# Optimization experiments

Measured on AMD Instinct MI355X. Metric: run time of the kernel, lower is better.

Reference implementation:

```python
import jax, jax.numpy as jnp
import numpy as np

N = 50000
E = 800000
EPS = 1e-5


def graph_conv(x, src, dst, ew, W_rel, b_rel, W_root):
    # PyG GraphConv (aggr='add'): lin_rel(sum_j e_ij * x_j) + lin_root(x_i)
    msg = x[src] * ew[:, None]                      # [E, F_in]
    agg = jax.ops.segment_sum(msg, dst, num_segments=N)  # [N, F_in]
    return agg @ W_rel.T + b_rel + x @ W_root.T


def batchnorm_relu(h, gamma, beta):
    mu = jnp.mean(h, axis=0)
    var = jnp.mean(jnp.square(h - mu), axis=0)
    hn = (h - mu) * jax.lax.rsqrt(var + EPS)
    return jax.nn.relu(hn * gamma + beta)


def setup_inputs() -> dict:
    key = jax.random.key(0)
    ks = jax.random.split(key, 16)
    d_in, h, d_out = 128, 256, 64

    def lin(k, fo, fi):
        return jax.random.normal(k, (fo, fi), jnp.float32) * (1.0 / np.sqrt(fi))

    return {
        "x": jax.random.normal(ks[0], (N, d_in), jnp.float32),
        "edge_index": jax.random.randint(ks[1], (2, E), 0, N, jnp.int32),
        "edge_weight": jax.random.uniform(ks[2], (E,), jnp.float32),
        "Wr0": lin(ks[3], h, d_in), "br0": jnp.zeros((h,), jnp.float32), "Wt0": lin(ks[4], h, d_in),
        "g0": jnp.ones((h,), jnp.float32), "be0": jnp.zeros((h,), jnp.float32),
        "Wr1": lin(ks[5], h, h), "br1": jnp.zeros((h,), jnp.float32), "Wt1": lin(ks[6], h, h),
        "g1": jnp.ones((h,), jnp.float32), "be1": jnp.zeros((h,), jnp.float32),
        "Wr2": lin(ks[7], d_out, h), "br2": jnp.zeros((d_out,), jnp.float32), "Wt2": lin(ks[8], d_out, h),
    }


def reference(x, edge_index, edge_weight, Wr0, br0, Wt0, g0, be0,
              Wr1, br1, Wt1, g1, be1, Wr2, br2, Wt2):
    src, dst = edge_index[0], edge_index[1]
    h = graph_conv(x, src, dst, edge_weight, Wr0, br0, Wt0)
    h = batchnorm_relu(h, g0, be0)
    h = graph_conv(h, src, dst, edge_weight, Wr1, br1, Wt1)
    h = batchnorm_relu(h, g1, be1)
    return graph_conv(h, src, dst, edge_weight, Wr2, br2, Wt2)
```

## Files before the change

### kernel.cpp

```cpp
#include <hip/hip_runtime.h>
#include <cstddef>
#include <cstdint>

#define SCAN_B 512

using bf16x8 = __attribute__((ext_vector_type(8))) short;
using f32x4  = __attribute__((ext_vector_type(4))) float;

__device__ __forceinline__ unsigned short f2bf(float f) {
    unsigned int u = __builtin_bit_cast(unsigned int, f);
    return (unsigned short)((u + 0x7FFFu + ((u >> 16) & 1u)) >> 16);
}
__device__ __forceinline__ float bf2f(unsigned short b) {
    unsigned int u = ((unsigned int)b) << 16;
    return __builtin_bit_cast(float, u);
}
__device__ __forceinline__ float i2f(int i) { return __builtin_bit_cast(float, i); }
__device__ __forceinline__ float u2f(unsigned int u) { return __builtin_bit_cast(float, u); }
__device__ __forceinline__ void gload_lds16(const void* g, void* l) {
    __builtin_amdgcn_global_load_lds((const __attribute__((address_space(1))) void*)g,
                                     (__attribute__((address_space(3))) void*)l, 16, 0, 0);
}

__global__ void hist_conv_k(const int* __restrict__ dst, int* __restrict__ counts,
                            int* __restrict__ rank, int E, int histBlocks,
                            const float* __restrict__ x, const float* __restrict__ Wr0,
                            const float* __restrict__ Wt0, const float* __restrict__ Wr1,
                            const float* __restrict__ Wt1, const float* __restrict__ Wr2,
                            const float* __restrict__ Wt2, unsigned short* __restrict__ x_bf,
                            unsigned short* __restrict__ Wr0b, unsigned short* __restrict__ Wt0b,
                            unsigned short* __restrict__ Wr1b, unsigned short* __restrict__ Wt1b,
                            unsigned short* __restrict__ Wr2b, unsigned short* __restrict__ Wt2b,
                            int n4x) {
    if ((int)blockIdx.x < histBlocks) {
        int e = blockIdx.x * 256 + threadIdx.x;
        if (e < E) rank[e] = atomicAdd(&counts[dst[e]], 1);
        return;
    }
    int j = (blockIdx.x - histBlocks) * 256 + threadIdx.x;
    const float* s;
    unsigned short* d;
    if (j < n4x) { s = x; d = x_bf; }
    else {
        j -= n4x;
        if (j < 8192) { s = Wr0; d = Wr0b; }
        else { j -= 8192;
        if (j < 8192) { s = Wt0; d = Wt0b; }
        else { j -= 8192;
        if (j < 16384) { s = Wr1; d = Wr1b; }
        else { j -= 16384;
        if (j < 16384) { s = Wt1; d = Wt1b; }
        else { j -= 16384;
        if (j < 4096) { s = Wr2; d = Wr2b; }
        else { j -= 4096;
        if (j >= 4096) return;
        s = Wt2; d = Wt2b; } } } } }
    }
    float4 v = reinterpret_cast<const float4*>(s)[j];
    ushort4 o;
    o.x = f2bf(v.x); o.y = f2bf(v.y); o.z = f2bf(v.z); o.w = f2bf(v.w);
    reinterpret_cast<ushort4*>(d)[j] = o;
}

__global__ void scan1_k(const int* __restrict__ counts, int* __restrict__ partial,
                        int* __restrict__ blocksum, int Nn) {
    __shared__ int sh[SCAN_B];
    int i = blockIdx.x * SCAN_B + threadIdx.x;
    int v = (i < Nn) ? counts[i] : 0;
    sh[threadIdx.x] = v;
    __syncthreads();
    for (int off = 1; off < SCAN_B; off <<= 1) {
        int t = (threadIdx.x >= (unsigned)off) ? sh[threadIdx.x - off] : 0;
        __syncthreads();
        sh[threadIdx.x] += t;
        __syncthreads();
    }
    if (i < Nn) partial[i] = sh[threadIdx.x];
    if (threadIdx.x == SCAN_B - 1) blocksum[blockIdx.x] = sh[threadIdx.x];
}

__global__ void scan2_k(int* __restrict__ blocksum, int nb) {
    __shared__ int sh[256];
    int v = (threadIdx.x < (unsigned)nb) ? blocksum[threadIdx.x] : 0;
    sh[threadIdx.x] = v;
    __syncthreads();
    for (int off = 1; off < 256; off <<= 1) {
        int t = (threadIdx.x >= (unsigned)off) ? sh[threadIdx.x - off] : 0;
        __syncthreads();
        sh[threadIdx.x] += t;
        __syncthreads();
    }
    if (threadIdx.x < (unsigned)nb) blocksum[threadIdx.x] = sh[threadIdx.x];
}

__global__ void scan3_k(const int* __restrict__ partial, const int* __restrict__ blocksum,
                        int* __restrict__ offsets, int Nn) {
    int i = blockIdx.x * SCAN_B + threadIdx.x;
    if (i >= Nn) return;
    int add = (blockIdx.x > 0) ? blocksum[blockIdx.x - 1] : 0;
    offsets[i + 1] = partial[i] + add;
    if (i == 0) offsets[0] = 0;
}

__global__ void fill2_k(const int* __restrict__ src, const int* __restrict__ dst,
                        const float* __restrict__ ew, const int* __restrict__ offsets,
                        const int* __restrict__ rank, int2* __restrict__ e_sw, int E) {
    int e = blockIdx.x * blockDim.x + threadIdx.x;
    if (e >= E) return;
    int d = dst[e];
    int pos = offsets[d] + rank[e];
    e_sw[pos] = make_int2(src[e], __builtin_bit_cast(int, ew[e]));
}

template<int F>
__global__ void gather_bf_k(const unsigned short* __restrict__ x, const int* __restrict__ offsets,
                            const int2* __restrict__ e_sw, unsigned short* __restrict__ agg, int Nn) {
    int wid = __builtin_amdgcn_readfirstlane((blockIdx.x * blockDim.x + threadIdx.x) >> 6);
    int lane = threadIdx.x & 63;
    if (wid >= Nn) return;
    int p = offsets[wid], end = offsets[wid + 1];
    const char* xb = (const char*)x;
    if constexpr (F == 256) {
        const unsigned loff = lane * 8u;
        float a0 = 0.f, a1 = 0.f, a2 = 0.f, a3 = 0.f;
        for (; p + 8 <= end; p += 8) {
            int2 ee[8];
            #pragma unroll
            for (int i = 0; i < 8; ++i) ee[i] = e_sw[p + i];
            uint2 vv[8];
            #pragma unroll
            for (int i = 0; i < 8; ++i)
                vv[i] = *reinterpret_cast<const uint2*>(xb + ((unsigned)ee[i].x * 512u + loff));
            #pragma unroll
            for (int i = 0; i < 8; ++i) {
                float w = i2f(ee[i].y);
                a0 += w * u2f(vv[i].x << 16); a1 += w * u2f(vv[i].x & 0xFFFF0000u);
                a2 += w * u2f(vv[i].y << 16); a3 += w * u2f(vv[i].y & 0xFFFF0000u);
            }
        }
        for (; p < end; ++p) {
            int2 e0 = e_sw[p];
            uint2 v0 = *reinterpret_cast<const uint2*>(xb + ((unsigned)e0.x * 512u + loff));
            float w = i2f(e0.y);
            a0 += w * u2f(v0.x << 16); a1 += w * u2f(v0.x & 0xFFFF0000u);
            a2 += w * u2f(v0.y << 16); a3 += w * u2f(v0.y & 0xFFFF0000u);
        }
        uint2 o;
        o.x = (unsigned)f2bf(a0) | ((unsigned)f2bf(a1) << 16);
        o.y = (unsigned)f2bf(a2) | ((unsigned)f2bf(a3) << 16);
        *reinterpret_cast<uint2*>(agg + (size_t)wid * 256 + lane * 4) = o;
    } else {
        const unsigned loff = lane * 4u;
        float a0 = 0.f, a1 = 0.f;
        for (; p + 8 <= end; p += 8) {
            int2 ee[8];
            #pragma unroll
            for (int i = 0; i < 8; ++i) ee[i] = e_sw[p + i];
            unsigned vv[8];
            #pragma unroll
            for (int i = 0; i < 8; ++i)
                vv[i] = *reinterpret_cast<const unsigned*>(xb + ((unsigned)ee[i].x * 256u + loff));
            #pragma unroll
            for (int i = 0; i < 8; ++i) {
                float w = i2f(ee[i].y);
                a0 += w * u2f(vv[i] << 16); a1 += w * u2f(vv[i] & 0xFFFF0000u);
            }
        }
        for (; p < end; ++p) {
            int2 e0 = e_sw[p];
            unsigned v0 = *reinterpret_cast<const unsigned*>(xb + ((unsigned)e0.x * 256u + loff));
            float w = i2f(e0.y);
            a0 += w * u2f(v0 << 16); a1 += w * u2f(v0 & 0xFFFF0000u);
        }
        unsigned o = (unsigned)f2bf(a0) | ((unsigned)f2bf(a1) << 16);
        *reinterpret_cast<unsigned*>(agg + (size_t)wid * 128 + lane * 2) = o;
    }
}

__global__ void gather_out_k(const unsigned short* __restrict__ t, const float* __restrict__ root,
                             const int* __restrict__ offsets, const int2* __restrict__ e_sw,
                             float* __restrict__ out, int Nn) {
    int gt = blockIdx.x * blockDim.x + threadIdx.x;
    int node = gt >> 4;
    int li = gt & 15;
    if (node >= Nn) return;
    int p = offsets[node], end = offsets[node + 1];
    const char* tb = (const char*)t;
    const unsigned loff = li * 8u;
    float a0 = 0.f, a1 = 0.f, a2 = 0.f, a3 = 0.f;
    for (; p + 8 <= end; p += 8) {
        int2 ee[8];
        #pragma unroll
        for (int i = 0; i < 8; ++i) ee[i] = e_sw[p + i];
        uint2 vv[8];
        #pragma unroll
        for (int i = 0; i < 8; ++i)
            vv[i] = *reinterpret_cast<const uint2*>(tb + ((unsigned)ee[i].x * 128u + loff));
        #pragma unroll
        for (int i = 0; i < 8; ++i) {
            float w = i2f(ee[i].y);
            a0 += w * u2f(vv[i].x << 16); a1 += w * u2f(vv[i].x & 0xFFFF0000u);
            a2 += w * u2f(vv[i].y << 16); a3 += w * u2f(vv[i].y & 0xFFFF0000u);
        }
    }
    for (; p < end; ++p) {
        int2 e0 = e_sw[p];
        uint2 v0 = *reinterpret_cast<const uint2*>(tb + ((unsigned)e0.x * 128u + loff));
        float w = i2f(e0.y);
        a0 += w * u2f(v0.x << 16); a1 += w * u2f(v0.x & 0xFFFF0000u);
        a2 += w * u2f(v0.y << 16); a3 += w * u2f(v0.y & 0xFFFF0000u);
    }
    float4 r = *reinterpret_cast<const float4*>(root + (size_t)node * 64 + li * 4);
    float4 o = make_float4(r.x + a0, r.y + a1, r.z + a2, r.w + a3);
    *reinterpret_cast<float4*>(out + (size_t)node * 64 + li * 4) = o;
}

template<int K, int O, int BM, int BN, int MODE>
__global__ __launch_bounds__(512, 4) void gemm_mfma_k(
        const unsigned short* __restrict__ A, const unsigned short* __restrict__ Wa,
        const unsigned short* __restrict__ X, const unsigned short* __restrict__ Wb,
        const float* __restrict__ bias, unsigned short* __restrict__ out_bf,
        float* __restrict__ out_f, float* __restrict__ sums, float* __restrict__ sumsq,
        int Nn) {
    constexpr int MI = BM / 32;
    constexpr int OJ = BN / 64;
    constexpr int KSTEPS = K / 64;
    constexpr int NT = (MODE == 0 ? 2 : 1) * KSTEPS;
    constexpr int ACH = BM / 64;
    constexpr int BCH = BN / 64;
    __shared__ unsigned short As[2][BM * 64];
    __shared__ unsigned short Bs[2][BN * 64];
    const int tid = threadIdx.x;
    const int w = tid >> 6, l = tid & 63;
    const int wr = w >> 2, wc = w & 3;
    const int lrow = l & 15, kgrp = l >> 4;
    int bx = blockIdx.x;
    bx = (bx & 7) * (gridDim.x >> 3) + (bx >> 3);
    const int m0 = bx * BM;
    const int n0 = blockIdx.y * BN;

    auto stage = [&](int buf, int t) {
        int ph = t / KSTEPS;
        int k0 = (t % KSTEPS) * 64;
        const unsigned short* Ap = (MODE == 0 && ph) ? X : A;
        const unsigned short* Wp = (MODE == 0 && ph) ? Wb : Wa;
        #pragma unroll
        for (int i = 0; i < ACH; ++i) {
            int c = i * 512 + tid;
            int row = c >> 3, slot = c & 7;
            gload_lds16(Ap + (size_t)(m0 + row) * K + k0 + ((slot ^ (row & 7)) << 3),
                        &As[buf][(i * 512 + w * 64) * 8]);
        }
        #pragma unroll
        for (int i = 0; i < BCH; ++i) {
            int c = i * 512 + tid;
            int row = c >> 3, slot = c & 7;
            gload_lds16(Wp + (size_t)(n0 + row) * K + k0 + ((slot ^ (row & 7)) << 3),
                        &Bs[buf][(i * 512 + w * 64) * 8]);
        }
    };

    f32x4 acc[MI][OJ];
    #pragma unroll
    for (int i = 0; i < MI; ++i)
        #pragma unroll
        for (int j = 0; j < OJ; ++j) {
            f32x4 z = {0.f, 0.f, 0.f, 0.f};
            acc[i][j] = z;
        }

    stage(0, 0);
    __syncthreads();
    #pragma unroll
    for (int t = 0; t < NT; ++t) {
        const int cur = t & 1;
        if (t + 1 < NT) stage(cur ^ 1, t + 1);
        #pragma unroll
        for (int ks = 0; ks < 2; ++ks) {
            bf16x8 a[MI], b[OJ];
            #pragma unroll
            for (int mi = 0; mi < MI; ++mi) {
                int row = wr * 64 + mi * 16 + lrow;
                int slot = (ks * 4 + kgrp) ^ (row & 7);
                a[mi] = *reinterpret_cast<const bf16x8*>(&As[cur][row * 64 + slot * 8]);
            }
            #pragma unroll
            for (int oj = 0; oj < OJ; ++oj) {
                int row = wc * 32 + oj * 16 + lrow;
                int slot = (ks * 4 + kgrp) ^ (row & 7);
                b[oj] = *reinterpret_cast<const bf16x8*>(&Bs[cur][row * 64 + slot * 8]);
            }
            #pragma unroll
            for (int mi = 0; mi < MI; ++mi)
                #pragma unroll
                for (int oj = 0; oj < OJ; ++oj)
                    acc[mi][oj] = __builtin_amdgcn_mfma_f32_16x16x32_bf16(
                        a[mi], b[oj], acc[mi][oj], 0, 0, 0);
        }
        __syncthreads();
    }

    if constexpr (MODE == 0) {
        #pragma unroll
        for (int oj = 0; oj < OJ; ++oj) {
            int col = n0 + wc * 32 + oj * 16 + lrow;
            float bcol = bias[col];
            float s = 0.f, q = 0.f;
            #pragma unroll
            for (int mi = 0; mi < MI; ++mi) {
                #pragma unroll
                for (int r = 0; r < 4; ++r) {
                    int row = m0 + wr * 64 + mi * 16 + kgrp * 4 + r;
                    float v = acc[mi][oj][r] + bcol;
                    if (row < Nn) {
                        out_bf[(size_t)row * O + col] = f2bf(v);
                        s += v; q += v * v;
                    }
                }
            }
            s += __shfl_xor(s, 16, 64); q += __shfl_xor(q, 16, 64);
            s += __shfl_xor(s, 32, 64); q += __shfl_xor(q, 32, 64);
            if (kgrp == 0) {
                atomicAdd(&sums[col], s);
                atomicAdd(&sumsq[col], q);
            }
        }
    } else {
        #pragma unroll
        for (int oj = 0; oj < OJ; ++oj) {
            int col = n0 + wc * 32 + oj * 16 + lrow;
            #pragma unroll
            for (int mi = 0; mi < MI; ++mi) {
                #pragma unroll
                for (int r = 0; r < 4; ++r) {
                    int row = m0 + wr * 64 + mi * 16 + kgrp * 4 + r;
                    if (row < Nn) {
                        if (col < 64)
                            out_bf[(size_t)row * 64 + col] = f2bf(acc[mi][oj][r]);
                        else
                            out_f[(size_t)row * 64 + (col - 64)] = acc[mi][oj][r] + bias[col - 64];
                    }
                }
            }
        }
    }
}

__global__ void bn_relu_bf_k(const unsigned short* __restrict__ h, const float* __restrict__ sums,
                             const float* __restrict__ sumsq, const float* __restrict__ g,
                             const float* __restrict__ be, unsigned short* __restrict__ hb,
                             float invN, int total4) {
    int t = blockIdx.x * blockDim.x + threadIdx.x;
    if (t >= total4) return;
    int f0 = (t & 63) * 4;
    float4 sm = *reinterpret_cast<const float4*>(sums + f0);
    float4 sq = *reinterpret_cast<const float4*>(sumsq + f0);
    float4 gg = *reinterpret_cast<const float4*>(g + f0);
    float4 bb = *reinterpret_cast<const float4*>(be + f0);
    float smv[4] = {sm.x, sm.y, sm.z, sm.w};
    float sqv[4] = {sq.x, sq.y, sq.z, sq.w};
    float ggv[4] = {gg.x, gg.y, gg.z, gg.w};
    float bbv[4] = {bb.x, bb.y, bb.z, bb.w};
    ushort4 v = reinterpret_cast<const ushort4*>(h)[t];
    unsigned short vv[4] = {v.x, v.y, v.z, v.w};
    ushort4 o;
    unsigned short* op = &o.x;
    #pragma unroll
    for (int c = 0; c < 4; ++c) {
        float mu = smv[c] * invN;
        float var = sqv[c] * invN - mu * mu;
        float sc = ggv[c] * rsqrtf(var + 1e-5f);
        float sh = bbv[c] - mu * sc;
        op[c] = f2bf(fmaxf(bf2f(vv[c]) * sc + sh, 0.f));
    }
    reinterpret_cast<ushort4*>(hb)[t] = o;
}

extern "C" void kernel_launch(void* const* d_in, const int* in_sizes, int n_in,
                              void* d_out, int out_size, void* d_ws, size_t ws_size,
                              hipStream_t stream) {
    const float* x   = (const float*)d_in[0];
    const int*   ei  = (const int*)d_in[1];
    const float* ew  = (const float*)d_in[2];
    const float* Wr0 = (const float*)d_in[3];
    const float* br0 = (const float*)d_in[4];
    const float* Wt0 = (const float*)d_in[5];
    const float* g0  = (const float*)d_in[6];
    const float* be0 = (const float*)d_in[7];
    const float* Wr1 = (const float*)d_in[8];
    const float* br1 = (const float*)d_in[9];
    const float* Wt1 = (const float*)d_in[10];
    const float* g1  = (const float*)d_in[11];
    const float* be1 = (const float*)d_in[12];
    const float* Wr2 = (const float*)d_in[13];
    const float* br2 = (const float*)d_in[14];
    const float* Wt2 = (const float*)d_in[15];

    const int E  = in_sizes[2];
    const int Nn = in_sizes[0] / 128;
    const size_t NP = 50176;
    const int* src = ei;
    const int* dst = ei + E;

    unsigned short* x_bf   = (unsigned short*)d_ws;
    unsigned short* agg_bf = x_bf + NP * 128;
    unsigned short* h0N    = agg_bf + NP * 256;
    unsigned short* h1N    = h0N + NP * 256;
    unsigned short* h_bf   = h1N + NP * 256;
    unsigned short* t_bf   = h_bf + NP * 256;
    unsigned short* wbf    = t_bf + NP * 64;
    unsigned short* Wr0b = wbf;
    unsigned short* Wt0b = wbf + 32768;
    unsigned short* Wr1b = wbf + 65536;
    unsigned short* Wt1b = wbf + 131072;
    unsigned short* W2cat = wbf + 196608;
    float* root  = (float*)(wbf + 229376);
    int2*  e_sw  = (int2*)(root + NP * 64);
    float* stats = (float*)(e_sw + E);
    int*   counts  = (int*)(stats + 4096);
    int*   partial = counts + Nn;
    int*   blocksum = partial + Nn;
    int*   rank    = blocksum + 512;
    int*   offsets = rank + E;

    dim3 blk(256);
    const int nbScan = (Nn + SCAN_B - 1) / SCAN_B;
    const float invN = 1.0f / (float)Nn;
    const int n4x = Nn * 32;
    const int histBlocks = (E + 255) / 256;
    const int convBlocks = (n4x + 57344 + 255) / 256;

    hipMemsetAsync(stats, 0, (4096 + (size_t)Nn) * sizeof(float), stream);

    hist_conv_k<<<dim3(histBlocks + convBlocks), blk, 0, stream>>>(
        dst, counts, rank, E, histBlocks,
        x, Wr0, Wt0, Wr1, Wt1, Wr2, Wt2,
        x_bf, Wr0b, Wt0b, Wr1b, Wt1b, W2cat, W2cat + 16384, n4x);
    scan1_k<<<dim3(nbScan), dim3(SCAN_B), 0, stream>>>(counts, partial, blocksum, Nn);
    scan2_k<<<dim3(1), dim3(256), 0, stream>>>(blocksum, nbScan);
    scan3_k<<<dim3(nbScan), dim3(SCAN_B), 0, stream>>>(partial, blocksum, offsets, Nn);
    fill2_k<<<dim3(histBlocks), blk, 0, stream>>>(src, dst, ew, offsets, rank, e_sw, E);

    const int gatherBlocks = (Nn * 64 + 255) / 256;

    gather_bf_k<128><<<dim3(gatherBlocks), blk, 0, stream>>>(x_bf, offsets, e_sw, agg_bf, Nn);
    gemm_mfma_k<128, 256, 128, 128, 0><<<dim3(NP / 128, 2), dim3(512), 0, stream>>>(
        agg_bf, Wr0b, x_bf, Wt0b, br0, h_bf, nullptr, stats + 0, stats + 256, Nn);
    bn_relu_bf_k<<<dim3((Nn * 64 + 255) / 256), blk, 0, stream>>>(
        h_bf, stats + 0, stats + 256, g0, be0, h0N, invN, Nn * 64);

    gather_bf_k<256><<<dim3(gatherBlocks), blk, 0, stream>>>(h0N, offsets, e_sw, agg_bf, Nn);
    gemm_mfma_k<256, 256, 128, 128, 0><<<dim3(NP / 128, 2), dim3(512), 0, stream>>>(
        agg_bf, Wr1b, h0N, Wt1b, br1, h_bf, nullptr, stats + 1024, stats + 1280, Nn);
    bn_relu_bf_k<<<dim3((Nn * 64 + 255) / 256), blk, 0, stream>>>(
        h_bf, stats + 1024, stats + 1280, g1, be1, h1N, invN, Nn * 64);

    gemm_mfma_k<256, 128, 128, 128, 1><<<dim3(NP / 128, 1), dim3(512), 0, stream>>>(
        h1N, W2cat, nullptr, nullptr, br2, t_bf, root, nullptr, nullptr, Nn);
    gather_out_k<<<dim3((Nn * 16 + 255) / 256), blk, 0, stream>>>(
        t_bf, root, offsets, e_sw, (float*)d_out, Nn);
}
```

Baseline: 304.6 us.

## Bucket CSR edges by source range and shrink GEMM K-tile to 32

The edge histogram now keys on (dst, src>>12), giving 16 sub-buckets per destination. The edge list is therefore sorted roughly by source within each destination row, which should improve gather locality and cache reuse. The scan grows to 16x the elements, so scan2 now loops in chunks of 256 with a carry. Separately, the MFMA GEMM K-step drops from 64 to 32, halving LDS use with a new swizzle, at the cost of more iterations and barriers.

```diff
diff --git a/kernel.cpp b/kernel.cpp
--- a/kernel.cpp
+++ b/kernel.cpp
@@ -3,6 +3,7 @@
 #include <cstdint>
 
 #define SCAN_B 512
+#define SBK 16
 
 using bf16x8 = __attribute__((ext_vector_type(8))) short;
 using f32x4  = __attribute__((ext_vector_type(4))) float;
@@ -22,8 +23,9 @@
                                      (__attribute__((address_space(3))) void*)l, 16, 0, 0);
 }
 
-__global__ void hist_conv_k(const int* __restrict__ dst, int* __restrict__ counts,
-                            int* __restrict__ rank, int E, int histBlocks,
+__global__ void hist_conv_k(const int* __restrict__ src, const int* __restrict__ dst,
+                            int* __restrict__ counts2, int* __restrict__ rank, int E,
+                            int histBlocks,
                             const float* __restrict__ x, const float* __restrict__ Wr0,
                             const float* __restrict__ Wt0, const float* __restrict__ Wr1,
                             const float* __restrict__ Wt1, const float* __restrict__ Wr2,
@@ -34,7 +36,7 @@
                             int n4x) {
     if ((int)blockIdx.x < histBlocks) {
         int e = blockIdx.x * 256 + threadIdx.x;
-        if (e < E) rank[e] = atomicAdd(&counts[dst[e]], 1);
+        if (e < E) rank[e] = atomicAdd(&counts2[dst[e] * SBK + (src[e] >> 12)], 1);
         return;
     }
     int j = (blockIdx.x - histBlocks) * 256 + threadIdx.x;
@@ -63,10 +65,10 @@
 }
 
 __global__ void scan1_k(const int* __restrict__ counts, int* __restrict__ partial,
-                        int* __restrict__ blocksum, int Nn) {
+                        int* __restrict__ blocksum, int M) {
     __shared__ int sh[SCAN_B];
     int i = blockIdx.x * SCAN_B + threadIdx.x;
-    int v = (i < Nn) ? counts[i] : 0;
+    int v = (i < M) ? counts[i] : 0;
     sh[threadIdx.x] = v;
     __syncthreads();
     for (int off = 1; off < SCAN_B; off <<= 1) {
@@ -75,50 +77,59 @@
         sh[threadIdx.x] += t;
         __syncthreads();
     }
-    if (i < Nn) partial[i] = sh[threadIdx.x];
+    if (i < M) partial[i] = sh[threadIdx.x];
     if (threadIdx.x == SCAN_B - 1) blocksum[blockIdx.x] = sh[threadIdx.x];
 }
 
 __global__ void scan2_k(int* __restrict__ blocksum, int nb) {
     __shared__ int sh[256];
-    int v = (threadIdx.x < (unsigned)nb) ? blocksum[threadIdx.x] : 0;
-    sh[threadIdx.x] = v;
+    __shared__ int carry_s;
+    if (threadIdx.x == 0) carry_s = 0;
     __syncthreads();
-    for (int off = 1; off < 256; off <<= 1) {
-        int t = (threadIdx.x >= (unsigned)off) ? sh[threadIdx.x - off] : 0;
-        __syncthreads();
-        sh[threadIdx.x] += t;
-        __syncthreads();
-    }
-    if (threadIdx.x < (unsigned)nb) blocksum[threadIdx.x] = sh[threadIdx.x];
+    for (int base = 0; base < nb; base += 256) {
+        int i = base + threadIdx.x;
+        int v = (i < nb) ? blocksum[i] : 0;
+        sh[threadIdx.x] = v;
+        __syncthreads();
+        for (int off = 1; off < 256; off <<= 1) {
+            int t = (threadIdx.x >= (unsigned)off) ? sh[threadIdx.x - off] : 0;
+            __syncthreads();
+            sh[threadIdx.x] += t;
+            __syncthreads();
+        }
+        if (i < nb) blocksum[i] = sh[threadIdx.x] + carry_s;
+        __syncthreads();
+        if (threadIdx.x == 0) carry_s += sh[255];
+        __syncthreads();
+    }
 }
 
 __global__ void scan3_k(const int* __restrict__ partial, const int* __restrict__ blocksum,
-                        int* __restrict__ offsets, int Nn) {
+                        int* __restrict__ offsets2, int M) {
     int i = blockIdx.x * SCAN_B + threadIdx.x;
-    if (i >= Nn) return;
+    if (i >= M) return;
     int add = (blockIdx.x > 0) ? blocksum[blockIdx.x - 1] : 0;
-    offsets[i + 1] = partial[i] + add;
-    if (i == 0) offsets[0] = 0;
+    offsets2[i + 1] = partial[i] + add;
+    if (i == 0) offsets2[0] = 0;
 }
 
 __global__ void fill2_k(const int* __restrict__ src, const int* __restrict__ dst,
-                        const float* __restrict__ ew, const int* __restrict__ offsets,
+                        const float* __restrict__ ew, const int* __restrict__ offsets2,
                         const int* __restrict__ rank, int2* __restrict__ e_sw, int E) {
     int e = blockIdx.x * blockDim.x + threadIdx.x;
     if (e >= E) return;
-    int d = dst[e];
-    int pos = offsets[d] + rank[e];
-    e_sw[pos] = make_int2(src[e], __builtin_bit_cast(int, ew[e]));
+    int s = src[e];
+    int pos = offsets2[dst[e] * SBK + (s >> 12)] + rank[e];
+    e_sw[pos] = make_int2(s, __builtin_bit_cast(int, ew[e]));
 }
 
 template<int F>
-__global__ void gather_bf_k(const unsigned short* __restrict__ x, const int* __restrict__ offsets,
+__global__ void gather_bf_k(const unsigned short* __restrict__ x, const int* __restrict__ offsets2,
                             const int2* __restrict__ e_sw, unsigned short* __restrict__ agg, int Nn) {
     int wid = __builtin_amdgcn_readfirstlane((blockIdx.x * blockDim.x + threadIdx.x) >> 6);
     int lane = threadIdx.x & 63;
     if (wid >= Nn) return;
-    int p = offsets[wid], end = offsets[wid + 1];
+    int p = offsets2[wid * SBK], end = offsets2[wid * SBK + SBK];
     const char* xb = (const char*)x;
     if constexpr (F == 256) {
         const unsigned loff = lane * 8u;
@@ -178,13 +189,13 @@
 }
 
 __global__ void gather_out_k(const unsigned short* __restrict__ t, const float* __restrict__ root,
-                             const int* __restrict__ offsets, const int2* __restrict__ e_sw,
+                             const int* __restrict__ offsets2, const int2* __restrict__ e_sw,
                              float* __restrict__ out, int Nn) {
     int gt = blockIdx.x * blockDim.x + threadIdx.x;
     int node = gt >> 4;
     int li = gt & 15;
     if (node >= Nn) return;
-    int p = offsets[node], end = offsets[node + 1];
+    int p = offsets2[node * SBK], end = offsets2[node * SBK + SBK];
     const char* tb = (const char*)t;
     const unsigned loff = li * 8u;
     float a0 = 0.f, a1 = 0.f, a2 = 0.f, a3 = 0.f;
@@ -215,21 +226,20 @@
     *reinterpret_cast<float4*>(out + (size_t)node * 64 + li * 4) = o;
 }
 
-template<int K, int O, int BM, int BN, int MODE>
+template<int K, int O, int MODE>
 __global__ __launch_bounds__(512, 4) void gemm_mfma_k(
         const unsigned short* __restrict__ A, const unsigned short* __restrict__ Wa,
         const unsigned short* __restrict__ X, const unsigned short* __restrict__ Wb,
         const float* __restrict__ bias, unsigned short* __restrict__ out_bf,
         float* __restrict__ out_f, float* __restrict__ sums, float* __restrict__ sumsq,
         int Nn) {
-    constexpr int MI = BM / 32;
-    constexpr int OJ = BN / 64;
-    constexpr int KSTEPS = K / 64;
+    constexpr int BM = 128, BN = 128;
+    constexpr int MI = 4;
+    constexpr int OJ = 2;
+    constexpr int KSTEPS = K / 32;
     constexpr int NT = (MODE == 0 ? 2 : 1) * KSTEPS;
-    constexpr int ACH = BM / 64;
-    constexpr int BCH = BN / 64;
-    __shared__ unsigned short As[2][BM * 64];
-    __shared__ unsigned short Bs[2][BN * 64];
+    __shared__ unsigned short As[2][BM * 32];
+    __shared__ unsigned short Bs[2][BN * 32];
     const int tid = threadIdx.x;
     const int w = tid >> 6, l = tid & 63;
     const int wr = w >> 2, wc = w & 3;
@@ -238,26 +248,16 @@
     bx = (bx & 7) * (gridDim.x >> 3) + (bx >> 3);
     const int m0 = bx * BM;
     const int n0 = blockIdx.y * BN;
+    const int srow = tid >> 2, sslot = tid & 3;
+    const int gslot = sslot ^ ((srow >> 1) & 3);
 
     auto stage = [&](int buf, int t) {
         int ph = t / KSTEPS;
-        int k0 = (t % KSTEPS) * 64;
+        int k0 = (t % KSTEPS) * 32;
         const unsigned short* Ap = (MODE == 0 && ph) ? X : A;
         const unsigned short* Wp = (MODE == 0 && ph) ? Wb : Wa;
-        #pragma unroll
-        for (int i = 0; i < ACH; ++i) {
-            int c = i * 512 + tid;
-            int row = c >> 3, slot = c & 7;
-            gload_lds16(Ap + (size_t)(m0 + row) * K + k0 + ((slot ^ (row & 7)) << 3),
-                        &As[buf][(i * 512 + w * 64) * 8]);
-        }
-        #pragma unroll
-        for (int i = 0; i < BCH; ++i) {
-            int c = i * 512 + tid;
-            int row = c >> 3, slot = c & 7;
-            gload_lds16(Wp + (size_t)(n0 + row) * K + k0 + ((slot ^ (row & 7)) << 3),
-                        &Bs[buf][(i * 512 + w * 64) * 8]);
-        }
+        gload_lds16(Ap + (size_t)(m0 + srow) * K + k0 + (gslot << 3), &As[buf][w * 512]);
+        gload_lds16(Wp + (size_t)(n0 + srow) * K + k0 + (gslot << 3), &Bs[buf][w * 512]);
     };
 
     f32x4 acc[MI][OJ];
@@ -275,28 +275,25 @@
     for (int t = 0; t < NT; ++t) {
         const int cur = t & 1;
         if (t + 1 < NT) stage(cur ^ 1, t + 1);
-        #pragma unroll
-        for (int ks = 0; ks < 2; ++ks) {
-            bf16x8 a[MI], b[OJ];
-            #pragma unroll
-            for (int mi = 0; mi < MI; ++mi) {
-                int row = wr * 64 + mi * 16 + lrow;
-                int slot = (ks * 4 + kgrp) ^ (row & 7);
-                a[mi] = *reinterpret_cast<const bf16x8*>(&As[cur][row * 64 + slot * 8]);
-            }
-            #pragma unroll
-            for (int oj = 0; oj < OJ; ++oj) {
-                int row = wc * 32 + oj * 16 + lrow;
-                int slot = (ks * 4 + kgrp) ^ (row & 7);
-                b[oj] = *reinterpret_cast<const bf16x8*>(&Bs[cur][row * 64 + slot * 8]);
-            }
-            #pragma unroll
-            for (int mi = 0; mi < MI; ++mi)
-                #pragma unroll
-                for (int oj = 0; oj < OJ; ++oj)
-                    acc[mi][oj] = __builtin_amdgcn_mfma_f32_16x16x32_bf16(
-                        a[mi], b[oj], acc[mi][oj], 0, 0, 0);
-        }
+        bf16x8 a[MI], b[OJ];
+        #pragma unroll
+        for (int mi = 0; mi < MI; ++mi) {
+            int row = wr * 64 + mi * 16 + lrow;
+            int slot = kgrp ^ ((row >> 1) & 3);
+            a[mi] = *reinterpret_cast<const bf16x8*>(&As[cur][row * 32 + slot * 8]);
+        }
+        #pragma unroll
+        for (int oj = 0; oj < OJ; ++oj) {
+            int row = wc * 32 + oj * 16 + lrow;
+            int slot = kgrp ^ ((row >> 1) & 3);
+            b[oj] = *reinterpret_cast<const bf16x8*>(&Bs[cur][row * 32 + slot * 8]);
+        }
+        #pragma unroll
+        for (int mi = 0; mi < MI; ++mi)
+            #pragma unroll
+            for (int oj = 0; oj < OJ; ++oj)
+                acc[mi][oj] = __builtin_amdgcn_mfma_f32_16x16x32_bf16(
+                    a[mi], b[oj], acc[mi][oj], 0, 0, 0);
         __syncthreads();
     }
 
@@ -399,6 +396,7 @@
     const int E  = in_sizes[2];
     const int Nn = in_sizes[0] / 128;
     const size_t NP = 50176;
+    const int  M  = Nn * SBK;
     const int* src = ei;
     const int* dst = ei + E;
 
@@ -417,46 +415,46 @@
     float* root  = (float*)(wbf + 229376);
     int2*  e_sw  = (int2*)(root + NP * 64);
     float* stats = (float*)(e_sw + E);
-    int*   counts  = (int*)(stats + 4096);
-    int*   partial = counts + Nn;
-    int*   blocksum = partial + Nn;
-    int*   rank    = blocksum + 512;
-    int*   offsets = rank + E;
+    int*   counts2 = (int*)(stats + 4096);
+    int*   partial = counts2 + M;
+    int*   blocksum = partial + M;
+    int*   rank    = blocksum + 2048;
+    int*   offsets2 = rank + E;
 
     dim3 blk(256);
-    const int nbScan = (Nn + SCAN_B - 1) / SCAN_B;
+    const int nbScan = (M + SCAN_B - 1) / SCAN_B;
     const float invN = 1.0f / (float)Nn;
     const int n4x = Nn * 32;
     const int histBlocks = (E + 255) / 256;
     const int convBlocks = (n4x + 57344 + 255) / 256;
 
-    hipMemsetAsync(stats, 0, (4096 + (size_t)Nn) * sizeof(float), stream);
+    hipMemsetAsync(stats, 0, (4096 + (size_t)M) * sizeof(float), stream);
 
     hist_conv_k<<<dim3(histBlocks + convBlocks), blk, 0, stream>>>(
-        dst, counts, rank, E, histBlocks,
+        src, dst, counts2, rank, E, histBlocks,
         x, Wr0, Wt0, Wr1, Wt1, Wr2, Wt2,
         x_bf, Wr0b, Wt0b, Wr1b, Wt1b, W2cat, W2cat + 16384, n4x);
-    scan1_k<<<dim3(nbScan), dim3(SCAN_B), 0, stream>>>(counts, partial, blocksum, Nn);
+    scan1_k<<<dim3(nbScan), dim3(SCAN_B), 0, stream>>>(counts2, partial, blocksum, M);
     scan2_k<<<dim3(1), dim3(256), 0, stream>>>(blocksum, nbScan);
-    scan3_k<<<dim3(nbScan), dim3(SCAN_B), 0, stream>>>(partial, blocksum, offsets, Nn);
-    fill2_k<<<dim3(histBlocks), blk, 0, stream>>>(src, dst, ew, offsets, rank, e_sw, E);
+    scan3_k<<<dim3(nbScan), dim3(SCAN_B), 0, stream>>>(partial, blocksum, offsets2, M);
+    fill2_k<<<dim3(histBlocks), blk, 0, stream>>>(src, dst, ew, offsets2, rank, e_sw, E);
 
     const int gatherBlocks = (Nn * 64 + 255) / 256;
 
-    gather_bf_k<128><<<dim3(gatherBlocks), blk, 0, stream>>>(x_bf, offsets, e_sw, agg_bf, Nn);
-    gemm_mfma_k<128, 256, 128, 128, 0><<<dim3(NP / 128, 2), dim3(512), 0, stream>>>(
+    gather_bf_k<128><<<dim3(gatherBlocks), blk, 0, stream>>>(x_bf, offsets2, e_sw, agg_bf, Nn);
+    gemm_mfma_k<128, 256, 0><<<dim3(NP / 128, 2), dim3(512), 0, stream>>>(
         agg_bf, Wr0b, x_bf, Wt0b, br0, h_bf, nullptr, stats + 0, stats + 256, Nn);
     bn_relu_bf_k<<<dim3((Nn * 64 + 255) / 256), blk, 0, stream>>>(
         h_bf, stats + 0, stats + 256, g0, be0, h0N, invN, Nn * 64);
 
-    gather_bf_k<256><<<dim3(gatherBlocks), blk, 0, stream>>>(h0N, offsets, e_sw, agg_bf, Nn);
-    gemm_mfma_k<256, 256, 128, 128, 0><<<dim3(NP / 128, 2), dim3(512), 0, stream>>>(
+    gather_bf_k<256><<<dim3(gatherBlocks), blk, 0, stream>>>(h0N, offsets2, e_sw, agg_bf, Nn);
+    gemm_mfma_k<256, 256, 0><<<dim3(NP / 128, 2), dim3(512), 0, stream>>>(
         agg_bf, Wr1b, h0N, Wt1b, br1, h_bf, nullptr, stats + 1024, stats + 1280, Nn);
     bn_relu_bf_k<<<dim3((Nn * 64 + 255) / 256), blk, 0, stream>>>(
         h_bf, stats + 1024, stats + 1280, g1, be1, h1N, invN, Nn * 64);
 
-    gemm_mfma_k<256, 128, 128, 128, 1><<<dim3(NP / 128, 1), dim3(512), 0, stream>>>(
+    gemm_mfma_k<256, 128, 1><<<dim3(NP / 128, 1), dim3(512), 0, stream>>>(
         h1N, W2cat, nullptr, nullptr, br2, t_bf, root, nullptr, nullptr, Nn);
     gather_out_k<<<dim3((Nn * 16 + 255) / 256), blk, 0, stream>>>(
-        t_bf, root, offsets, e_sw, (float*)d_out, Nn);
-}
+        t_bf, root, offsets2, e_sw, (float*)d_out, Nn);
+}
```

Measured after the change: 315.8 us. 1.04x slower.
